# Performance work log

Hardware: AMD Instinct MI355X
Metric: run time of the kernel (lower is better)

The kernel has to match this reference:

```python
import jax, jax.numpy as jnp
import numpy as np

B, C, T, E = 8, 512, 2048, 512
LN_EPS = 1e-5


def setup_inputs() -> dict:
    key = jax.random.key(0)
    ks = jax.random.split(key, 12)
    std = 0.02
    return {
        "x": jax.random.normal(ks[0], (B, C, T), dtype=jnp.float32),
        "Wq": jax.random.normal(ks[1], (C, E), dtype=jnp.float32) * std,
        "bq": jnp.zeros((E,), dtype=jnp.float32),
        "Wk": jax.random.normal(ks[2], (C, E), dtype=jnp.float32) * std,
        "bk": jnp.zeros((E,), dtype=jnp.float32),
        "Wv": jax.random.normal(ks[3], (C, E), dtype=jnp.float32) * std,
        "bv": jnp.zeros((E,), dtype=jnp.float32),
        "Wo": jax.random.normal(ks[4], (E, C), dtype=jnp.float32) * std,
        "bo": jnp.zeros((C,), dtype=jnp.float32),
        "gamma": jnp.ones((C,), dtype=jnp.float32),
        "beta": jnp.zeros((C,), dtype=jnp.float32),
    }


def reference(x, Wq, bq, Wk, bk, Wv, bv, Wo, bo, gamma, beta):
    # x: [B, C, T] channels-first -> residual [B, T, C]
    residual = jnp.transpose(x, (0, 2, 1))
    q = residual @ Wq + bq            # [B, T, E]
    k = residual @ Wk + bk            # [B, T, E]
    v = residual @ Wv + bv            # [B, T, E]
    # Unscaled dot-product attention (no 1/sqrt(E) in the original)
    energy = jnp.einsum("bte,bse->bts", q, k)         # [B, T, T]
    attn = jax.nn.softmax(energy, axis=-1)             # [B, T, T]
    attended = jnp.einsum("bts,bse->bte", attn, v)    # [B, T, E]
    attended = attended @ Wo + bo                      # [B, T, C]
    h = attended + residual                            # residual add
    # LayerNorm over last dim (C)
    mu = jnp.mean(h, axis=-1, keepdims=True)
    var = jnp.mean(jnp.square(h - mu), axis=-1, keepdims=True)
    out = (h - mu) * jax.lax.rsqrt(var + LN_EPS) * gamma + beta
    return attn, out
```

## Files before the change

### kernel.cpp

```cpp
#include <hip/hip_runtime.h>

#define B_ 8
#define C_ 512
#define T_ 2048
#define E_ 512
#define LN_EPS 1e-5f

typedef __attribute__((ext_vector_type(8))) short bf16x8;
typedef __attribute__((ext_vector_type(4))) float f32x4;

__device__ __forceinline__ unsigned short f2bf(float f) {
  union { float f; unsigned u; } v; v.f = f;
  unsigned u = v.u;
  u += 0x7fff + ((u >> 16) & 1);
  return (unsigned short)(u >> 16);
}
__device__ __forceinline__ float bf2f(unsigned short h) {
  union { unsigned u; float f; } v; v.u = ((unsigned)h) << 16;
  return v.f;
}

__device__ __forceinline__ void gl2lds16(const unsigned short* g, unsigned short* l) {
  __builtin_amdgcn_global_load_lds(
      (const __attribute__((address_space(1))) unsigned int*)g,
      (__attribute__((address_space(3))) unsigned int*)l, 16, 0, 0);
}

__global__ __launch_bounds__(256) void transpose_x(const float* __restrict__ x,
    unsigned short* __restrict__ rb) {
  __shared__ float tile[32][33];
  int b = blockIdx.z;
  int t0 = blockIdx.x * 32, c0 = blockIdx.y * 32;
  int tx = threadIdx.x, ty = threadIdx.y;
  const float* xb = x + (long)b * C_ * T_;
#pragma unroll
  for (int i = 0; i < 4; i++)
    tile[ty + i * 8][tx] = xb[(long)(c0 + ty + i * 8) * T_ + t0 + tx];
  __syncthreads();
  long ob = (long)b * T_ * C_;
#pragma unroll
  for (int i = 0; i < 4; i++)
    rb[ob + (long)(t0 + ty + i * 8) * C_ + c0 + tx] = f2bf(tile[tx][ty + i * 8]);
}

__global__ __launch_bounds__(256) void transpose_w(const float* __restrict__ W,
    unsigned short* __restrict__ Wt) {
  __shared__ float tile[32][33];
  int e0 = blockIdx.x * 32, c0 = blockIdx.y * 32;
  int tx = threadIdx.x, ty = threadIdx.y;
#pragma unroll
  for (int i = 0; i < 4; i++)
    tile[ty + i * 8][tx] = W[(long)(c0 + ty + i * 8) * E_ + e0 + tx];
  __syncthreads();
#pragma unroll
  for (int i = 0; i < 4; i++)
    Wt[(long)(e0 + ty + i * 8) * C_ + c0 + tx] = f2bf(tile[tx][ty + i * 8]);
}

__global__ void concat_bias(const float* __restrict__ bq, const float* __restrict__ bk,
                            float* __restrict__ bqk) {
  int i = blockIdx.x * 256 + threadIdx.x;
  bqk[i] = (i < 512) ? bq[i] : bk[i - 512];
}

template<int EPI, int BM>
__global__ __launch_bounds__(256) void gemm_bt(
    const unsigned short* __restrict__ Ap, const unsigned short* __restrict__ Btp,
    unsigned short* __restrict__ Cp, const float* __restrict__ bias,
    const unsigned short* __restrict__ resid,
    int K, int lda, int ldb, int ldc, long sA, long sB, long sC) {
  __shared__ unsigned short As[BM * 64];
  __shared__ unsigned short Bs[128 * 64];
  constexpr int WI = BM / 32;
  const int b = blockIdx.z;
  const int tid = threadIdx.x;
  const int lane = tid & 63, wave = tid >> 6;
  const int wr = (wave >> 1) * (BM / 2);
  const int wc = (wave & 1) * 64;
  const int quad = lane >> 4, l16 = lane & 15;
  const long m0 = (long)blockIdx.y * BM, n0 = (long)blockIdx.x * 128;

  const int srow = lane >> 3;
  const int gcol = ((lane & 7) ^ srow) * 8;
  const unsigned short* ga = Ap + (long)b * sA + (m0 + srow) * (long)lda + gcol;
  const unsigned short* gb = Btp + (long)b * sB + (n0 + srow) * (long)ldb + gcol;

  f32x4 acc[WI][4] = {};

  for (int k0 = 0; k0 < K; k0 += 64) {
    __syncthreads();
#pragma unroll
    for (int s = 0; s < WI; s++)
      gl2lds16(ga + (s * 32 + wave * 8) * (long)lda + k0, &As[(s * 32 + wave * 8) * 64]);
#pragma unroll
    for (int s = 0; s < 4; s++)
      gl2lds16(gb + (s * 32 + wave * 8) * (long)ldb + k0, &Bs[(s * 32 + wave * 8) * 64]);
    __syncthreads();
#pragma unroll
    for (int ks = 0; ks < 2; ks++) {
      const int cs = ((ks * 4 + quad) ^ (l16 & 7)) * 8;
      bf16x8 af[WI], bfr[4];
#pragma unroll
      for (int i = 0; i < WI; i++)
        af[i] = *(const bf16x8*)&As[(wr + i * 16 + l16) * 64 + cs];
#pragma unroll
      for (int j = 0; j < 4; j++)
        bfr[j] = *(const bf16x8*)&Bs[(wc + j * 16 + l16) * 64 + cs];
#pragma unroll
      for (int i = 0; i < WI; i++)
#pragma unroll
        for (int j = 0; j < 4; j++)
          acc[i][j] = __builtin_amdgcn_mfma_f32_16x16x32_bf16(af[i], bfr[j], acc[i][j], 0, 0, 0);
    }
  }

  const long cb = (long)b * sC;
#pragma unroll
  for (int i = 0; i < WI; i++) {
#pragma unroll
    for (int rr = 0; rr < 4; rr++) {
      const long m = m0 + wr + i * 16 + quad * 4 + rr;
#pragma unroll
      for (int j = 0; j < 4; j++) {
        const long n = n0 + wc + j * 16 + l16;
        float v = acc[i][j][rr];
        if (EPI == 0) v += bias[n];
        else if (EPI == 1) v += bias[m];
        else if (EPI == 2) v += bias[n] + bf2f(resid[m * (long)ldc + n]);
        Cp[cb + m * (long)ldc + n] = f2bf(v);
      }
    }
  }
}

__global__ __launch_bounds__(256) void softmax_rows(unsigned short* __restrict__ eb,
                                                    float* __restrict__ attn) {
  long row = blockIdx.x;
  unsigned short* p = eb + row * (long)T_;
  float* o = attn + row * (long)T_;
  int tid = threadIdx.x;
  bf16x8 raw = *(const bf16x8*)(p + tid * 8);
  float vals[8];
  float mx = -1e30f;
#pragma unroll
  for (int i = 0; i < 8; i++) {
    vals[i] = bf2f((unsigned short)raw[i]);
    mx = fmaxf(mx, vals[i]);
  }
#pragma unroll
  for (int o2 = 32; o2 > 0; o2 >>= 1) mx = fmaxf(mx, __shfl_xor(mx, o2, 64));
  __shared__ float red[4];
  if ((tid & 63) == 0) red[tid >> 6] = mx;
  __syncthreads();
  mx = fmaxf(fmaxf(red[0], red[1]), fmaxf(red[2], red[3]));
  float sum = 0.f;
#pragma unroll
  for (int i = 0; i < 8; i++) { vals[i] = __expf(vals[i] - mx); sum += vals[i]; }
#pragma unroll
  for (int o2 = 32; o2 > 0; o2 >>= 1) sum += __shfl_xor(sum, o2, 64);
  __shared__ float red2[4];
  if ((tid & 63) == 0) red2[tid >> 6] = sum;
  __syncthreads();
  sum = red2[0] + red2[1] + red2[2] + red2[3];
  float inv = 1.f / sum;
  unsigned short ob[8];
  float r0[4], r1[4];
#pragma unroll
  for (int i = 0; i < 8; i++) {
    float r = vals[i] * inv;
    if (i < 4) r0[i] = r; else r1[i - 4] = r;
    ob[i] = f2bf(r);
  }
  *(float4*)(o + tid * 8)     = *(float4*)r0;
  *(float4*)(o + tid * 8 + 4) = *(float4*)r1;
  *(bf16x8*)(p + tid * 8) = *(bf16x8*)ob;
}

__global__ __launch_bounds__(256) void layernorm_rows(const unsigned short* __restrict__ hb,
    const float* __restrict__ gamma, const float* __restrict__ beta,
    float* __restrict__ out) {
  long row = blockIdx.x;
  const unsigned short* p = hb + row * C_;
  int tid = threadIdx.x;
  unsigned pr = *(const unsigned*)(p + 2 * tid);
  float v0 = bf2f((unsigned short)(pr & 0xffff));
  float v1 = bf2f((unsigned short)(pr >> 16));
  float s = v0 + v1, sq = v0 * v0 + v1 * v1;
#pragma unroll
  for (int o = 32; o > 0; o >>= 1) { s += __shfl_xor(s, o, 64); sq += __shfl_xor(sq, o, 64); }
  __shared__ float rs[4], rq[4];
  if ((tid & 63) == 0) { rs[tid >> 6] = s; rq[tid >> 6] = sq; }
  __syncthreads();
  s = rs[0] + rs[1] + rs[2] + rs[3];
  sq = rq[0] + rq[1] + rq[2] + rq[3];
  float mu = s * (1.f / 512.f);
  float var = sq * (1.f / 512.f) - mu * mu;
  float rstd = rsqrtf(var + LN_EPS);
  out[row * C_ + 2 * tid]     = (v0 - mu) * rstd * gamma[2 * tid] + beta[2 * tid];
  out[row * C_ + 2 * tid + 1] = (v1 - mu) * rstd * gamma[2 * tid + 1] + beta[2 * tid + 1];
}

extern "C" void kernel_launch(void* const* d_in, const int* in_sizes, int n_in,
                              void* d_out, int out_size, void* d_ws, size_t ws_size,
                              hipStream_t stream) {
  const float* x  = (const float*)d_in[0];
  const float* Wq = (const float*)d_in[1];
  const float* bq = (const float*)d_in[2];
  const float* Wk = (const float*)d_in[3];
  const float* bk = (const float*)d_in[4];
  const float* Wv = (const float*)d_in[5];
  const float* bv = (const float*)d_in[6];
  const float* Wo = (const float*)d_in[7];
  const float* bo = (const float*)d_in[8];
  const float* gamma = (const float*)d_in[9];
  const float* beta  = (const float*)d_in[10];
  float* out = (float*)d_out;

  char* ws = (char*)d_ws;
  unsigned short* res_b = (unsigned short*)ws;
  unsigned short* qk    = (unsigned short*)(ws + (16ul << 20));
  unsigned short* att   = (unsigned short*)(ws + (16ul << 20));
  unsigned short* hb    = (unsigned short*)(ws + (32ul << 20));
  unsigned short* vt    = (unsigned short*)(ws + (48ul << 20));
  unsigned short* eb    = (unsigned short*)(ws + (64ul << 20));
  unsigned short* WqkT  = (unsigned short*)(ws + (128ul << 20));
  unsigned short* WvT   = (unsigned short*)(ws + (130ul << 20));
  unsigned short* WoT   = (unsigned short*)(ws + (130ul << 20) + 524288);
  float*          bqk   = (float*)(ws + (131ul << 20));

  float* attn_f = out;
  float* outln  = out + (long)B_ * T_ * T_;

  dim3 tb(32, 8);
  transpose_x<<<dim3(T_ / 32, C_ / 32, B_), tb, 0, stream>>>(x, res_b);
  transpose_w<<<dim3(16, 16), tb, 0, stream>>>(Wq, WqkT);
  transpose_w<<<dim3(16, 16), tb, 0, stream>>>(Wk, WqkT + 512 * 512);
  transpose_w<<<dim3(16, 16), tb, 0, stream>>>(Wv, WvT);
  transpose_w<<<dim3(16, 16), tb, 0, stream>>>(Wo, WoT);
  concat_bias<<<dim3(4), 256, 0, stream>>>(bq, bk, bqk);

  gemm_bt<0, 128><<<dim3(8, 128, 1), 256, 0, stream>>>(
      res_b, WqkT, qk, bqk, nullptr, 512, 512, 512, 1024, 0L, 0L, 0L);
  gemm_bt<1, 64><<<dim3(16, 8, B_), 256, 0, stream>>>(
      WvT, res_b, vt, bv, nullptr, 512, 512, 512, 2048,
      0L, (long)T_ * C_, 512L * 2048);
  gemm_bt<4, 128><<<dim3(16, 16, B_), 256, 0, stream>>>(
      qk, qk + 512, eb, nullptr, nullptr, 512, 1024, 1024, 2048,
      (long)T_ * 1024, (long)T_ * 1024, (long)T_ * T_);
  softmax_rows<<<dim3(B_ * T_), 256, 0, stream>>>(eb, attn_f);
  gemm_bt<4, 64><<<dim3(4, 32, B_), 256, 0, stream>>>(
      eb, vt, att, nullptr, nullptr, 2048, 2048, 2048, 512,
      (long)T_ * T_, 512L * 2048, (long)T_ * 512);
  gemm_bt<2, 64><<<dim3(4, 256, 1), 256, 0, stream>>>(
      att, WoT, hb, bo, res_b, 512, 512, 512, 512, 0L, 0L, 0L);
  layernorm_rows<<<dim3(B_ * T_), 256, 0, stream>>>(hb, gamma, beta, outln);
}
```

Baseline: 423.7 us.

## Fuse softmax into QK epilogue stats and PV prologue, merge weight transposes

The QK^T GEMM epilogue now computes per-tile row max and sum-of-exp partials, and a small kernel combines them into final per-row statistics. The PV GEMM then normalizes the stored bf16 logits while loading its A tiles, and only the x-index-0 blocks write the fp32 attention output. This removes the standalone softmax pass, including its rewrite of the bf16 logit buffer. The cost is recomputing exp in each of the four PV column blocks and a less efficient register-staged A-tile load. The four weight transposes are also merged into one launch.

Result: slower. 465.0 us (+9.8%).

```diff
diff --git a/kernel.cpp b/kernel.cpp
--- a/kernel.cpp
+++ b/kernel.cpp
@@ -43,9 +43,16 @@
     rb[ob + (long)(t0 + ty + i * 8) * C_ + c0 + tx] = f2bf(tile[tx][ty + i * 8]);
 }
 
-__global__ __launch_bounds__(256) void transpose_w(const float* __restrict__ W,
-    unsigned short* __restrict__ Wt) {
+__global__ __launch_bounds__(256) void transpose_w4(
+    const float* __restrict__ Wq, const float* __restrict__ Wk,
+    const float* __restrict__ Wv, const float* __restrict__ Wo,
+    unsigned short* __restrict__ WqkT, unsigned short* __restrict__ WvT,
+    unsigned short* __restrict__ WoT) {
   __shared__ float tile[32][33];
+  int z = blockIdx.z;
+  const float* W = (z == 0) ? Wq : (z == 1) ? Wk : (z == 2) ? Wv : Wo;
+  unsigned short* D = (z == 0) ? WqkT : (z == 1) ? (WqkT + 512 * 512)
+                     : (z == 2) ? WvT : WoT;
   int e0 = blockIdx.x * 32, c0 = blockIdx.y * 32;
   int tx = threadIdx.x, ty = threadIdx.y;
 #pragma unroll
@@ -54,7 +61,7 @@
   __syncthreads();
 #pragma unroll
   for (int i = 0; i < 4; i++)
-    Wt[(long)(e0 + ty + i * 8) * C_ + c0 + tx] = f2bf(tile[tx][ty + i * 8]);
+    D[(long)(e0 + ty + i * 8) * C_ + c0 + tx] = f2bf(tile[tx][ty + i * 8]);
 }
 
 __global__ void concat_bias(const float* __restrict__ bq, const float* __restrict__ bk,
@@ -67,10 +74,11 @@
 __global__ __launch_bounds__(256) void gemm_bt(
     const unsigned short* __restrict__ Ap, const unsigned short* __restrict__ Btp,
     unsigned short* __restrict__ Cp, const float* __restrict__ bias,
-    const unsigned short* __restrict__ resid,
+    const unsigned short* __restrict__ resid, float2* __restrict__ statsp,
     int K, int lda, int ldb, int ldc, long sA, long sB, long sC) {
   __shared__ unsigned short As[BM * 64];
   __shared__ unsigned short Bs[128 * 64];
+  __shared__ float2 sred[(EPI == 5) ? 128 : 1][2];
   constexpr int WI = BM / 32;
   const int b = blockIdx.z;
   const int tid = threadIdx.x;
@@ -120,60 +128,149 @@
 #pragma unroll
     for (int rr = 0; rr < 4; rr++) {
       const long m = m0 + wr + i * 16 + quad * 4 + rr;
+      if constexpr (EPI == 5) {
+        float vv[4];
+        float mx = -1e30f;
+#pragma unroll
+        for (int j = 0; j < 4; j++) {
+          const long n = n0 + wc + j * 16 + l16;
+          unsigned short ub = f2bf(acc[i][j][rr]);
+          Cp[cb + m * (long)ldc + n] = ub;
+          vv[j] = bf2f(ub);
+          mx = fmaxf(mx, vv[j]);
+        }
+        float sm = 0.f;
+#pragma unroll
+        for (int j = 0; j < 4; j++) sm += __expf(vv[j] - mx);
+#pragma unroll
+        for (int o = 1; o < 16; o <<= 1) {
+          float om = __shfl_xor(mx, o, 64);
+          float os = __shfl_xor(sm, o, 64);
+          float nm = fmaxf(mx, om);
+          sm = sm * __expf(mx - nm) + os * __expf(om - nm);
+          mx = nm;
+        }
+        if (l16 == 0) sred[wr + i * 16 + quad * 4 + rr][wave & 1] = make_float2(mx, sm);
+      } else {
+#pragma unroll
+        for (int j = 0; j < 4; j++) {
+          const long n = n0 + wc + j * 16 + l16;
+          float v = acc[i][j][rr];
+          if (EPI == 0) v += bias[n];
+          else if (EPI == 1) v += bias[m];
+          else if (EPI == 2) v += bias[n] + bf2f(resid[m * (long)ldc + n]);
+          Cp[cb + m * (long)ldc + n] = f2bf(v);
+        }
+      }
+    }
+  }
+  if constexpr (EPI == 5) {
+    __syncthreads();
+    if (tid < 128) {
+      float2 a0 = sred[tid][0], a1 = sred[tid][1];
+      float M = fmaxf(a0.x, a1.x);
+      float S = a0.y * __expf(a0.x - M) + a1.y * __expf(a1.x - M);
+      statsp[((long)b * T_ + m0 + tid) * 16 + blockIdx.x] = make_float2(M, S);
+    }
+  }
+}
+
+__global__ __launch_bounds__(256) void combine_stats(const float2* __restrict__ sp,
+                                                     float2* __restrict__ rs) {
+  long row = blockIdx.x * 256L + threadIdx.x;
+  const float2* p = sp + row * 16;
+  float M = -1e30f;
+#pragma unroll
+  for (int i = 0; i < 16; i++) M = fmaxf(M, p[i].x);
+  float S = 0.f;
+#pragma unroll
+  for (int i = 0; i < 16; i++) S += p[i].y * __expf(p[i].x - M);
+  rs[row] = make_float2(M, 1.f / S);
+}
+
+__global__ __launch_bounds__(256) void pv_fused(
+    const unsigned short* __restrict__ eb, const unsigned short* __restrict__ vt,
+    const float2* __restrict__ rowstats, float* __restrict__ attn_f,
+    unsigned short* __restrict__ att) {
+  __shared__ unsigned short As[64 * 64];
+  __shared__ unsigned short Bs[128 * 64];
+  const int b = blockIdx.z;
+  const int tid = threadIdx.x;
+  const int lane = tid & 63, wave = tid >> 6;
+  const int wr = (wave >> 1) * 32, wc = (wave & 1) * 64;
+  const int quad = lane >> 4, l16 = lane & 15;
+  const long m0 = (long)blockIdx.y * 64, n0 = (long)blockIdx.x * 128;
+  const bool writer = (blockIdx.x == 0);
+
+  const int srow = lane >> 3;
+  const int gcolB = ((lane & 7) ^ srow) * 8;
+  const unsigned short* gb = vt + (long)b * 512 * 2048 + (n0 + srow) * 2048L + gcolB;
+
+  const int ar = tid >> 2;
+  const int pg0 = tid & 3;
+  const long arow = (long)b * T_ + m0 + ar;
+  const unsigned short* ga = eb + arow * (long)T_ + pg0 * 8;
+  float* fo = attn_f + arow * (long)T_ + pg0 * 8;
+  const float2 st = rowstats[arow];
+  const float negM = -st.x, inv = st.y;
+  const int pL0 = (pg0 ^ (ar & 7)) * 8;
+  const int pL1 = ((pg0 + 4) ^ (ar & 7)) * 8;
+
+  f32x4 acc[2][4] = {};
+
+  for (int k0 = 0; k0 < T_; k0 += 64) {
+    __syncthreads();
+#pragma unroll
+    for (int s = 0; s < 4; s++)
+      gl2lds16(gb + (s * 32 + wave * 8) * 2048L + k0, &Bs[(s * 32 + wave * 8) * 64]);
+    bf16x8 r0 = *(const bf16x8*)(ga + k0);
+    bf16x8 r1 = *(const bf16x8*)(ga + k0 + 32);
+    unsigned short p0[8], p1[8];
+    float f0[8], f1[8];
+#pragma unroll
+    for (int j = 0; j < 8; j++) {
+      float pa = __expf(bf2f((unsigned short)r0[j]) + negM) * inv;
+      f0[j] = pa; p0[j] = f2bf(pa);
+      float pb = __expf(bf2f((unsigned short)r1[j]) + negM) * inv;
+      f1[j] = pb; p1[j] = f2bf(pb);
+    }
+    if (writer) {
+      *(float4*)(fo + k0)      = *(float4*)&f0[0];
+      *(float4*)(fo + k0 + 4)  = *(float4*)&f0[4];
+      *(float4*)(fo + k0 + 32) = *(float4*)&f1[0];
+      *(float4*)(fo + k0 + 36) = *(float4*)&f1[4];
+    }
+    *(bf16x8*)&As[ar * 64 + pL0] = *(bf16x8*)p0;
+    *(bf16x8*)&As[ar * 64 + pL1] = *(bf16x8*)p1;
+    __syncthreads();
+#pragma unroll
+    for (int ks = 0; ks < 2; ks++) {
+      const int cs = ((ks * 4 + quad) ^ (l16 & 7)) * 8;
+      bf16x8 af[2], bfr[4];
+      af[0] = *(const bf16x8*)&As[(wr + l16) * 64 + cs];
+      af[1] = *(const bf16x8*)&As[(wr + 16 + l16) * 64 + cs];
+#pragma unroll
+      for (int j = 0; j < 4; j++)
+        bfr[j] = *(const bf16x8*)&Bs[(wc + j * 16 + l16) * 64 + cs];
+#pragma unroll
+      for (int i = 0; i < 2; i++)
+#pragma unroll
+        for (int j = 0; j < 4; j++)
+          acc[i][j] = __builtin_amdgcn_mfma_f32_16x16x32_bf16(af[i], bfr[j], acc[i][j], 0, 0, 0);
+    }
+  }
+
+#pragma unroll
+  for (int i = 0; i < 2; i++)
+#pragma unroll
+    for (int rr = 0; rr < 4; rr++) {
+      const long m = m0 + wr + i * 16 + quad * 4 + rr;
 #pragma unroll
       for (int j = 0; j < 4; j++) {
         const long n = n0 + wc + j * 16 + l16;
-        float v = acc[i][j][rr];
-        if (EPI == 0) v += bias[n];
-        else if (EPI == 1) v += bias[m];
-        else if (EPI == 2) v += bias[n] + bf2f(resid[m * (long)ldc + n]);
-        Cp[cb + m * (long)ldc + n] = f2bf(v);
+        att[((long)b * T_ + m) * 512 + n] = f2bf(acc[i][j][rr]);
       }
     }
-  }
-}
-
-__global__ __launch_bounds__(256) void softmax_rows(unsigned short* __restrict__ eb,
-                                                    float* __restrict__ attn) {
-  long row = blockIdx.x;
-  unsigned short* p = eb + row * (long)T_;
-  float* o = attn + row * (long)T_;
-  int tid = threadIdx.x;
-  bf16x8 raw = *(const bf16x8*)(p + tid * 8);
-  float vals[8];
-  float mx = -1e30f;
-#pragma unroll
-  for (int i = 0; i < 8; i++) {
-    vals[i] = bf2f((unsigned short)raw[i]);
-    mx = fmaxf(mx, vals[i]);
-  }
-#pragma unroll
-  for (int o2 = 32; o2 > 0; o2 >>= 1) mx = fmaxf(mx, __shfl_xor(mx, o2, 64));
-  __shared__ float red[4];
-  if ((tid & 63) == 0) red[tid >> 6] = mx;
-  __syncthreads();
-  mx = fmaxf(fmaxf(red[0], red[1]), fmaxf(red[2], red[3]));
-  float sum = 0.f;
-#pragma unroll
-  for (int i = 0; i < 8; i++) { vals[i] = __expf(vals[i] - mx); sum += vals[i]; }
-#pragma unroll
-  for (int o2 = 32; o2 > 0; o2 >>= 1) sum += __shfl_xor(sum, o2, 64);
-  __shared__ float red2[4];
-  if ((tid & 63) == 0) red2[tid >> 6] = sum;
-  __syncthreads();
-  sum = red2[0] + red2[1] + red2[2] + red2[3];
-  float inv = 1.f / sum;
-  unsigned short ob[8];
-  float r0[4], r1[4];
-#pragma unroll
-  for (int i = 0; i < 8; i++) {
-    float r = vals[i] * inv;
-    if (i < 4) r0[i] = r; else r1[i - 4] = r;
-    ob[i] = f2bf(r);
-  }
-  *(float4*)(o + tid * 8)     = *(float4*)r0;
-  *(float4*)(o + tid * 8 + 4) = *(float4*)r1;
-  *(bf16x8*)(p + tid * 8) = *(bf16x8*)ob;
 }
 
 __global__ __launch_bounds__(256) void layernorm_rows(const unsigned short* __restrict__ hb,
@@ -227,31 +324,28 @@
   unsigned short* WvT   = (unsigned short*)(ws + (130ul << 20));
   unsigned short* WoT   = (unsigned short*)(ws + (130ul << 20) + 524288);
   float*          bqk   = (float*)(ws + (131ul << 20));
+  float2* statsp   = (float2*)(ws + (128ul << 20));
+  float2* rowstats = (float2*)(ws + (130ul << 20));
 
   float* attn_f = out;
   float* outln  = out + (long)B_ * T_ * T_;
 
   dim3 tb(32, 8);
   transpose_x<<<dim3(T_ / 32, C_ / 32, B_), tb, 0, stream>>>(x, res_b);
-  transpose_w<<<dim3(16, 16), tb, 0, stream>>>(Wq, WqkT);
-  transpose_w<<<dim3(16, 16), tb, 0, stream>>>(Wk, WqkT + 512 * 512);
-  transpose_w<<<dim3(16, 16), tb, 0, stream>>>(Wv, WvT);
-  transpose_w<<<dim3(16, 16), tb, 0, stream>>>(Wo, WoT);
+  transpose_w4<<<dim3(16, 16, 4), tb, 0, stream>>>(Wq, Wk, Wv, Wo, WqkT, WvT, WoT);
   concat_bias<<<dim3(4), 256, 0, stream>>>(bq, bk, bqk);
 
   gemm_bt<0, 128><<<dim3(8, 128, 1), 256, 0, stream>>>(
-      res_b, WqkT, qk, bqk, nullptr, 512, 512, 512, 1024, 0L, 0L, 0L);
+      res_b, WqkT, qk, bqk, nullptr, nullptr, 512, 512, 512, 1024, 0L, 0L, 0L);
   gemm_bt<1, 64><<<dim3(16, 8, B_), 256, 0, stream>>>(
-      WvT, res_b, vt, bv, nullptr, 512, 512, 512, 2048,
+      WvT, res_b, vt, bv, nullptr, nullptr, 512, 512, 512, 2048,
       0L, (long)T_ * C_, 512L * 2048);
-  gemm_bt<4, 128><<<dim3(16, 16, B_), 256, 0, stream>>>(
-      qk, qk + 512, eb, nullptr, nullptr, 512, 1024, 1024, 2048,
+  gemm_bt<5, 128><<<dim3(16, 16, B_), 256, 0, stream>>>(
+      qk, qk + 512, eb, nullptr, nullptr, statsp, 512, 1024, 1024, 2048,
       (long)T_ * 1024, (long)T_ * 1024, (long)T_ * T_);
-  softmax_rows<<<dim3(B_ * T_), 256, 0, stream>>>(eb, attn_f);
-  gemm_bt<4, 64><<<dim3(4, 32, B_), 256, 0, stream>>>(
-      eb, vt, att, nullptr, nullptr, 2048, 2048, 2048, 512,
-      (long)T_ * T_, 512L * 2048, (long)T_ * 512);
+  combine_stats<<<dim3(64), 256, 0, stream>>>(statsp, rowstats);
+  pv_fused<<<dim3(4, 32, B_), 256, 0, stream>>>(eb, vt, rowstats, attn_f, att);
   gemm_bt<2, 64><<<dim3(4, 256, 1), 256, 0, stream>>>(
-      att, WoT, hb, bo, res_b, 512, 512, 512, 512, 0L, 0L, 0L);
+      att, WoT, hb, bo, res_b, nullptr, 512, 512, 512, 512, 0L, 0L, 0L);
   layernorm_rows<<<dim3(B_ * T_), 256, 0, stream>>>(hb, gamma, beta, outln);
 }
```
